# Kernel tuning notes

Measured on AMD Instinct MI355X. Metric: run time of the kernel, lower is better.

The kernel has to match this reference:

```python
import jax, jax.numpy as jnp
import numpy as np

N_NODES = 500_000
N_EDGES = 500_000
H = 128  # hidden_channels


def setup_inputs() -> dict:
    key = jax.random.key(0)
    k = jax.random.split(key, 8)
    z = jax.random.normal(k[0], (N_NODES, H), dtype=jnp.float32)
    edge_index = jax.random.randint(k[1], (2, N_EDGES), 0, N_NODES, dtype=jnp.int64)
    s1 = 1.0 / np.sqrt(4 * H)
    s2 = 1.0 / np.sqrt(H)
    s3 = 1.0 / np.sqrt(H // 2)
    W1 = jax.random.uniform(k[2], (4 * H, H), jnp.float32, -s1, s1)
    b1 = jax.random.uniform(k[3], (H,), jnp.float32, -s1, s1)
    W2 = jax.random.uniform(k[4], (H, H // 2), jnp.float32, -s2, s2)
    b2 = jax.random.uniform(k[5], (H // 2,), jnp.float32, -s2, s2)
    W3 = jax.random.uniform(k[6], (H // 2, 1), jnp.float32, -s3, s3)
    b3 = jax.random.uniform(k[7], (1,), jnp.float32, -s3, s3)
    return {"z": z, "edge_index": edge_index,
            "W1": W1, "b1": b1, "W2": W2, "b2": b2, "W3": W3, "b3": b3}


def reference(z, edge_index, W1, b1, W2, b2, W3, b3):
    # gather endpoint embeddings: [E, H]
    src = z[edge_index[0]]
    dst = z[edge_index[1]]
    interaction = src * dst
    difference = jnp.abs(src - dst)
    edge_repr = jnp.concatenate([src, dst, interaction, difference], axis=-1)  # [E, 4H]
    # MLP decoder (dropout = identity at eval)
    h = jax.nn.relu(edge_repr @ W1 + b1)
    h = jax.nn.relu(h @ W2 + b2)
    score = (h @ W3 + b3).squeeze(-1)  # [E]
    return score
```

## Files before the change

### kernel.cpp

```cpp
#include <hip/hip_runtime.h>
#include <stdint.h>


typedef __bf16 bf16x8 __attribute__((ext_vector_type(8)));
typedef __bf16 bf16x4 __attribute__((ext_vector_type(4)));
typedef float  f32x4  __attribute__((ext_vector_type(4)));

__device__ __forceinline__ short f2bf(float f) {
    union { float f; uint32_t u; } v; v.f = f;
    uint32_t u = v.u;
    uint32_t r = (u + 0x7fffu + ((u >> 16) & 1u)) >> 16;
    return (short)r;
}

__global__ void prep_kernel(const float* __restrict__ W1, const float* __restrict__ W2,
                            short* __restrict__ stage1, short* __restrict__ stage2) {
    int idx = blockIdx.x * 256 + threadIdx.x;
    if (idx < 65536) {
        int k = idx >> 7, n = idx & 127;
        float v = W1[idx];
        int ntile = n >> 4, ln = n & 15;
        int kstep = k >> 5, kr = k & 31;
        int lane = (kr >> 3) * 16 + ln;
        int j = kr & 7;
        stage1[(((ntile * 16 + kstep) * 64 + lane) << 3) + j] = f2bf(v);
    } else if (idx < 65536 + 8192) {
        int i2 = idx - 65536;
        int k = i2 >> 6, n = i2 & 63;
        float v = W2[i2];
        int ntile = n >> 4, ln = n & 15;
        int kstep = k >> 5, kr = k & 31;
        int lane = (kr >> 3) * 16 + ln;
        int j = kr & 7;
        stage2[(((ntile * 4 + kstep) * 64 + lane) << 3) + j] = f2bf(v);
    }
}

__launch_bounds__(256, 4)
__global__ void link_kernel(const float* __restrict__ z,
                            const int*   __restrict__ ei,
                            const float* __restrict__ b1,
                            const float* __restrict__ b2,
                            const float* __restrict__ w3,
                            const float* __restrict__ b3,
                            const short* __restrict__ stage1,
                            const short* __restrict__ stage2,
                            float* __restrict__ out,
                            int E) {
    __shared__ __align__(16) char smem[32768];

    const int tid  = threadIdx.x;
    const int lane = tid & 63;
    const int wave = tid >> 6;
    const int ln15 = lane & 15;
    const int quad = lane >> 4;
    const int e0   = blockIdx.x * 64;

    const int c    = tid & 31;
    const int mrow = tid >> 5;
    int si[8], di[8];
    #pragma unroll
    for (int i = 0; i < 8; ++i) {
        int eg = e0 + mrow + i * 8;
        int egc = eg < E ? eg : (E - 1);
        si[i] = ei[egc];
        di[i] = ei[E + egc];
    }
    f32x4 sv[8], dv[8];
    #pragma unroll
    for (int i = 0; i < 8; ++i) {
        sv[i] = *(const f32x4*)(z + (size_t)si[i] * 128 + c * 4);
        dv[i] = *(const f32x4*)(z + (size_t)di[i] * 128 + c * 4);
    }
    const int cc   = c >> 1;
    const int half = c & 1;
    #pragma unroll
    for (int i = 0; i < 8; ++i) {
        int m = mrow + i * 8;
        int addr = m * 256 + ((cc ^ (m & 15)) << 4) + half * 8;
        bf16x4 ps, pd;
        #pragma unroll
        for (int j = 0; j < 4; ++j) { ps[j] = (__bf16)sv[i][j]; pd[j] = (__bf16)dv[i][j]; }
        *(bf16x4*)(smem + addr)         = ps;
        *(bf16x4*)(smem + 16384 + addr) = pd;
    }
    __syncthreads();

    f32x4 acc[4][2];
    #pragma unroll
    for (int mt = 0; mt < 4; ++mt)
        #pragma unroll
        for (int nt = 0; nt < 2; ++nt)
            acc[mt][nt] = (f32x4){0.f, 0.f, 0.f, 0.f};

    #pragma unroll
    for (int ks4 = 0; ks4 < 4; ++ks4) {
        bf16x8 Bs[2], Bd[2];
        #pragma unroll
        for (int nt = 0; nt < 2; ++nt) {
            int ntile = wave * 2 + nt;
            Bs[nt] = *(const bf16x8*)(stage1 + (((ntile * 16 + 0 + ks4) * 64 + lane) << 3));
            Bd[nt] = *(const bf16x8*)(stage1 + (((ntile * 16 + 4 + ks4) * 64 + lane) << 3));
        }
        #pragma unroll
        for (int mt = 0; mt < 4; ++mt) {
            int m = mt * 16 + ln15;
            int off = m * 256 + (((ks4 * 4 + quad) ^ (m & 15)) << 4);
            bf16x8 sf = *(const bf16x8*)(smem + off);
            bf16x8 df = *(const bf16x8*)(smem + 16384 + off);
            #pragma unroll
            for (int nt = 0; nt < 2; ++nt) {
                acc[mt][nt] = __builtin_amdgcn_mfma_f32_16x16x32_bf16(sf, Bs[nt], acc[mt][nt], 0, 0, 0);
                acc[mt][nt] = __builtin_amdgcn_mfma_f32_16x16x32_bf16(df, Bd[nt], acc[mt][nt], 0, 0, 0);
            }
        }
    }
    __syncthreads();

    {
        int mder = wave * 16 + ln15;
        #pragma unroll
        for (int ks4 = 0; ks4 < 4; ++ks4) {
            int addr = mder * 256 + (((ks4 * 4 + quad) ^ ln15) << 4);
            bf16x8 s = *(const bf16x8*)(smem + addr);
            bf16x8 d = *(const bf16x8*)(smem + 16384 + addr);
            bf16x8 it, dd;
            #pragma unroll
            for (int j = 0; j < 8; ++j) {
                float fs = (float)s[j], fd = (float)d[j];
                it[j] = (__bf16)(fs * fd);
                dd[j] = (__bf16)__builtin_fabsf(fs - fd);
            }
            *(bf16x8*)(smem + addr)         = it;
            *(bf16x8*)(smem + 16384 + addr) = dd;
        }
    }
    __syncthreads();

    #pragma unroll
    for (int ks4 = 0; ks4 < 4; ++ks4) {
        bf16x8 Bi[2], Bf[2];
        #pragma unroll
        for (int nt = 0; nt < 2; ++nt) {
            int ntile = wave * 2 + nt;
            Bi[nt] = *(const bf16x8*)(stage1 + (((ntile * 16 +  8 + ks4) * 64 + lane) << 3));
            Bf[nt] = *(const bf16x8*)(stage1 + (((ntile * 16 + 12 + ks4) * 64 + lane) << 3));
        }
        #pragma unroll
        for (int mt = 0; mt < 4; ++mt) {
            int m = mt * 16 + ln15;
            int off = m * 256 + (((ks4 * 4 + quad) ^ (m & 15)) << 4);
            bf16x8 itf = *(const bf16x8*)(smem + off);
            bf16x8 ddf = *(const bf16x8*)(smem + 16384 + off);
            #pragma unroll
            for (int nt = 0; nt < 2; ++nt) {
                acc[mt][nt] = __builtin_amdgcn_mfma_f32_16x16x32_bf16(itf, Bi[nt], acc[mt][nt], 0, 0, 0);
                acc[mt][nt] = __builtin_amdgcn_mfma_f32_16x16x32_bf16(ddf, Bf[nt], acc[mt][nt], 0, 0, 0);
            }
        }
    }
    __syncthreads();

    #pragma unroll
    for (int nt = 0; nt < 2; ++nt) {
        int n = (wave * 2 + nt) * 16 + ln15;
        float bias = b1[n];
        #pragma unroll
        for (int mt = 0; mt < 4; ++mt) {
            #pragma unroll
            for (int r = 0; r < 4; ++r) {
                int row = mt * 16 + quad * 4 + r;
                float h = acc[mt][nt][r] + bias;
                h = h > 0.f ? h : 0.f;
                int addr = row * 256 + (((n >> 3) ^ (row & 15)) << 4) + (n & 7) * 2;
                *(short*)(smem + addr) = f2bf(h);
            }
        }
    }
    __syncthreads();

    f32x4 acc2[4];
    #pragma unroll
    for (int mt = 0; mt < 4; ++mt) acc2[mt] = (f32x4){0.f, 0.f, 0.f, 0.f};

    #pragma unroll
    for (int ks = 0; ks < 4; ++ks) {
        bf16x8 b = *(const bf16x8*)(stage2 + (((wave * 4 + ks) * 64 + lane) << 3));
        #pragma unroll
        for (int mt = 0; mt < 4; ++mt) {
            int m = mt * 16 + ln15;
            int ccr = ks * 4 + quad;
            bf16x8 a = *(const bf16x8*)(smem + m * 256 + ((ccr ^ (m & 15)) << 4));
            acc2[mt] = __builtin_amdgcn_mfma_f32_16x16x32_bf16(a, b, acc2[mt], 0, 0, 0);
        }
    }
    __syncthreads();

    {
        int n2 = wave * 16 + ln15;
        float bias = b2[n2];
        #pragma unroll
        for (int mt = 0; mt < 4; ++mt) {
            #pragma unroll
            for (int r = 0; r < 4; ++r) {
                int row = mt * 16 + quad * 4 + r;
                float h = acc2[mt][r] + bias;
                h = h > 0.f ? h : 0.f;
                *(float*)(smem + row * 272 + n2 * 4) = h;
            }
        }
    }
    __syncthreads();

    if (wave == 0) {
        int e = lane;
        float accf = b3[0];
        const float* h2p = (const float*)(smem + e * 272);
        #pragma unroll
        for (int kk = 0; kk < 16; ++kk) {
            f32x4 h = *(const f32x4*)(h2p + kk * 4);
            f32x4 w = *(const f32x4*)(w3 + kk * 4);
            accf += h[0] * w[0] + h[1] * w[1] + h[2] * w[2] + h[3] * w[3];
        }
        if (e0 + e < E) out[e0 + e] = accf;
    }
}

extern "C" void kernel_launch(void* const* d_in, const int* in_sizes, int n_in,
                              void* d_out, int out_size, void* d_ws, size_t ws_size,
                              hipStream_t stream) {
    const float* z  = (const float*)d_in[0];
    const int*   ei = (const int*)  d_in[1];
    const float* W1 = (const float*)d_in[2];
    const float* b1 = (const float*)d_in[3];
    const float* W2 = (const float*)d_in[4];
    const float* b2 = (const float*)d_in[5];
    const float* W3 = (const float*)d_in[6];
    const float* b3 = (const float*)d_in[7];
    float* out = (float*)d_out;

    int E = in_sizes[1] / 2;

    short* stage1 = (short*)d_ws;
    short* stage2 = stage1 + 65536;

    prep_kernel<<<288, 256, 0, stream>>>(W1, W2, stage1, stage2);

    int nblk = (E + 63) / 64;
    link_kernel<<<nblk, 256, 0, stream>>>(z, ei, b1, b2, W3, b3, stage1, stage2, out, E);
}
```

Measured before the change: 415.3 us.

## Make link kernel persistent and prefetch next tile's gathers during compute

The edge MLP kernel becomes a persistent grid-stride loop over 64-edge tiles, launched with at most 768 blocks. While the current tile is being computed, it loads the next tile's edge indices and gathers its endpoint embeddings into registers, so gather latency overlaps MFMA work. Biases and W3 are cached in shared memory, and some syncthreads calls become explicit waitcnt plus barrier. This raises register pressure, which is why the occupancy hint drops from 4 to 3 blocks per CU, and fewer resident waves are left to hide latency.

Measured after the change: 939.2 us. 2.26x slower.

```diff
diff --git a/kernel.cpp b/kernel.cpp
--- a/kernel.cpp
+++ b/kernel.cpp
@@ -36,7 +36,7 @@
     }
 }
 
-__launch_bounds__(256, 4)
+__launch_bounds__(256, 3)
 __global__ void link_kernel(const float* __restrict__ z,
                             const int*   __restrict__ ei,
                             const float* __restrict__ b1,
@@ -46,183 +46,228 @@
                             const short* __restrict__ stage1,
                             const short* __restrict__ stage2,
                             float* __restrict__ out,
-                            int E) {
+                            int E, int ntiles) {
     __shared__ __align__(16) char smem[32768];
+    __shared__ __align__(16) float sbias[260];
 
     const int tid  = threadIdx.x;
     const int lane = tid & 63;
     const int wave = tid >> 6;
     const int ln15 = lane & 15;
     const int quad = lane >> 4;
-    const int e0   = blockIdx.x * 64;
+    const int G    = gridDim.x;
+
+    if (tid < 128)      sbias[tid] = b1[tid];
+    else if (tid < 192) sbias[tid] = b2[tid - 128];
+    else                sbias[tid] = w3[tid - 192];
+    if (tid == 0) sbias[256] = b3[0];
 
     const int c    = tid & 31;
     const int mrow = tid >> 5;
-    int si[8], di[8];
-    #pragma unroll
-    for (int i = 0; i < 8; ++i) {
-        int eg = e0 + mrow + i * 8;
-        int egc = eg < E ? eg : (E - 1);
-        si[i] = ei[egc];
-        di[i] = ei[E + egc];
-    }
-    f32x4 sv[8], dv[8];
-    #pragma unroll
-    for (int i = 0; i < 8; ++i) {
-        sv[i] = *(const f32x4*)(z + (size_t)si[i] * 128 + c * 4);
-        dv[i] = *(const f32x4*)(z + (size_t)di[i] * 128 + c * 4);
-    }
     const int cc   = c >> 1;
     const int half = c & 1;
-    #pragma unroll
-    for (int i = 0; i < 8; ++i) {
-        int m = mrow + i * 8;
-        int addr = m * 256 + ((cc ^ (m & 15)) << 4) + half * 8;
-        bf16x4 ps, pd;
-        #pragma unroll
-        for (int j = 0; j < 4; ++j) { ps[j] = (__bf16)sv[i][j]; pd[j] = (__bf16)dv[i][j]; }
-        *(bf16x4*)(smem + addr)         = ps;
-        *(bf16x4*)(smem + 16384 + addr) = pd;
+
+    int si[8], di[8];
+    f32x4 sv[8], dv[8];
+
+    int T = blockIdx.x;
+    {
+        int e0 = T * 64;
+        #pragma unroll
+        for (int i = 0; i < 8; ++i) {
+            int eg = e0 + mrow + i * 8;
+            int egc = eg < E ? eg : (E - 1);
+            si[i] = ei[egc];
+            di[i] = ei[E + egc];
+        }
+        #pragma unroll
+        for (int i = 0; i < 8; ++i) {
+            sv[i] = *(const f32x4*)(z + (size_t)si[i] * 128 + c * 4);
+            dv[i] = *(const f32x4*)(z + (size_t)di[i] * 128 + c * 4);
+        }
     }
-    __syncthreads();
-
-    f32x4 acc[4][2];
-    #pragma unroll
-    for (int mt = 0; mt < 4; ++mt)
-        #pragma unroll
-        for (int nt = 0; nt < 2; ++nt)
-            acc[mt][nt] = (f32x4){0.f, 0.f, 0.f, 0.f};
-
-    #pragma unroll
-    for (int ks4 = 0; ks4 < 4; ++ks4) {
-        bf16x8 Bs[2], Bd[2];
+
+    for (; T < ntiles; T += G) {
+        const int e0 = T * 64;
+        const bool hasNext = (T + G) < ntiles;
+
+        #pragma unroll
+        for (int i = 0; i < 8; ++i) {
+            int m = mrow + i * 8;
+            int addr = m * 256 + ((cc ^ (m & 15)) << 4) + half * 8;
+            bf16x4 ps, pd;
+            #pragma unroll
+            for (int j = 0; j < 4; ++j) { ps[j] = (__bf16)sv[i][j]; pd[j] = (__bf16)dv[i][j]; }
+            *(bf16x4*)(smem + addr)         = ps;
+            *(bf16x4*)(smem + 16384 + addr) = pd;
+        }
+        __syncthreads();
+
+        if (hasNext) {
+            int en0 = (T + G) * 64;
+            #pragma unroll
+            for (int i = 0; i < 8; ++i) {
+                int eg = en0 + mrow + i * 8;
+                int egc = eg < E ? eg : (E - 1);
+                si[i] = ei[egc];
+                di[i] = ei[E + egc];
+            }
+        }
+
+        f32x4 acc[4][2];
+        #pragma unroll
+        for (int mt = 0; mt < 4; ++mt)
+            #pragma unroll
+            for (int nt = 0; nt < 2; ++nt)
+                acc[mt][nt] = (f32x4){0.f, 0.f, 0.f, 0.f};
+
+        #pragma unroll
+        for (int ks4 = 0; ks4 < 4; ++ks4) {
+            bf16x8 Bs[2], Bd[2];
+            #pragma unroll
+            for (int nt = 0; nt < 2; ++nt) {
+                int ntile = wave * 2 + nt;
+                Bs[nt] = *(const bf16x8*)(stage1 + (((ntile * 16 + 0 + ks4) * 64 + lane) << 3));
+                Bd[nt] = *(const bf16x8*)(stage1 + (((ntile * 16 + 4 + ks4) * 64 + lane) << 3));
+            }
+            #pragma unroll
+            for (int mt = 0; mt < 4; ++mt) {
+                int m = mt * 16 + ln15;
+                int off = m * 256 + (((ks4 * 4 + quad) ^ (m & 15)) << 4);
+                bf16x8 sf = *(const bf16x8*)(smem + off);
+                bf16x8 df = *(const bf16x8*)(smem + 16384 + off);
+                #pragma unroll
+                for (int nt = 0; nt < 2; ++nt) {
+                    acc[mt][nt] = __builtin_amdgcn_mfma_f32_16x16x32_bf16(sf, Bs[nt], acc[mt][nt], 0, 0, 0);
+                    acc[mt][nt] = __builtin_amdgcn_mfma_f32_16x16x32_bf16(df, Bd[nt], acc[mt][nt], 0, 0, 0);
+                }
+            }
+        }
+        __syncthreads();
+
+        {
+            int mder = wave * 16 + ln15;
+            #pragma unroll
+            for (int ks4 = 0; ks4 < 4; ++ks4) {
+                int addr = mder * 256 + (((ks4 * 4 + quad) ^ ln15) << 4);
+                bf16x8 s = *(const bf16x8*)(smem + addr);
+                bf16x8 d = *(const bf16x8*)(smem + 16384 + addr);
+                bf16x8 it, dd;
+                #pragma unroll
+                for (int j = 0; j < 8; ++j) {
+                    float fs = (float)s[j], fd = (float)d[j];
+                    it[j] = (__bf16)(fs * fd);
+                    dd[j] = (__bf16)__builtin_fabsf(fs - fd);
+                }
+                *(bf16x8*)(smem + addr)         = it;
+                *(bf16x8*)(smem + 16384 + addr) = dd;
+            }
+        }
+        __syncthreads();
+
+        #pragma unroll
+        for (int ks4 = 0; ks4 < 4; ++ks4) {
+            bf16x8 Bi[2], Bf[2];
+            #pragma unroll
+            for (int nt = 0; nt < 2; ++nt) {
+                int ntile = wave * 2 + nt;
+                Bi[nt] = *(const bf16x8*)(stage1 + (((ntile * 16 +  8 + ks4) * 64 + lane) << 3));
+                Bf[nt] = *(const bf16x8*)(stage1 + (((ntile * 16 + 12 + ks4) * 64 + lane) << 3));
+            }
+            #pragma unroll
+            for (int mt = 0; mt < 4; ++mt) {
+                int m = mt * 16 + ln15;
+                int off = m * 256 + (((ks4 * 4 + quad) ^ (m & 15)) << 4);
+                bf16x8 itf = *(const bf16x8*)(smem + off);
+                bf16x8 ddf = *(const bf16x8*)(smem + 16384 + off);
+                #pragma unroll
+                for (int nt = 0; nt < 2; ++nt) {
+                    acc[mt][nt] = __builtin_amdgcn_mfma_f32_16x16x32_bf16(itf, Bi[nt], acc[mt][nt], 0, 0, 0);
+                    acc[mt][nt] = __builtin_amdgcn_mfma_f32_16x16x32_bf16(ddf, Bf[nt], acc[mt][nt], 0, 0, 0);
+                }
+            }
+        }
+        __syncthreads();
+
         #pragma unroll
         for (int nt = 0; nt < 2; ++nt) {
-            int ntile = wave * 2 + nt;
-            Bs[nt] = *(const bf16x8*)(stage1 + (((ntile * 16 + 0 + ks4) * 64 + lane) << 3));
-            Bd[nt] = *(const bf16x8*)(stage1 + (((ntile * 16 + 4 + ks4) * 64 + lane) << 3));
-        }
-        #pragma unroll
-        for (int mt = 0; mt < 4; ++mt) {
-            int m = mt * 16 + ln15;
-            int off = m * 256 + (((ks4 * 4 + quad) ^ (m & 15)) << 4);
-            bf16x8 sf = *(const bf16x8*)(smem + off);
-            bf16x8 df = *(const bf16x8*)(smem + 16384 + off);
-            #pragma unroll
-            for (int nt = 0; nt < 2; ++nt) {
-                acc[mt][nt] = __builtin_amdgcn_mfma_f32_16x16x32_bf16(sf, Bs[nt], acc[mt][nt], 0, 0, 0);
-                acc[mt][nt] = __builtin_amdgcn_mfma_f32_16x16x32_bf16(df, Bd[nt], acc[mt][nt], 0, 0, 0);
-            }
-        }
-    }
-    __syncthreads();
-
-    {
-        int mder = wave * 16 + ln15;
-        #pragma unroll
-        for (int ks4 = 0; ks4 < 4; ++ks4) {
-            int addr = mder * 256 + (((ks4 * 4 + quad) ^ ln15) << 4);
-            bf16x8 s = *(const bf16x8*)(smem + addr);
-            bf16x8 d = *(const bf16x8*)(smem + 16384 + addr);
-            bf16x8 it, dd;
-            #pragma unroll
-            for (int j = 0; j < 8; ++j) {
-                float fs = (float)s[j], fd = (float)d[j];
-                it[j] = (__bf16)(fs * fd);
-                dd[j] = (__bf16)__builtin_fabsf(fs - fd);
-            }
-            *(bf16x8*)(smem + addr)         = it;
-            *(bf16x8*)(smem + 16384 + addr) = dd;
-        }
-    }
-    __syncthreads();
-
-    #pragma unroll
-    for (int ks4 = 0; ks4 < 4; ++ks4) {
-        bf16x8 Bi[2], Bf[2];
-        #pragma unroll
-        for (int nt = 0; nt < 2; ++nt) {
-            int ntile = wave * 2 + nt;
-            Bi[nt] = *(const bf16x8*)(stage1 + (((ntile * 16 +  8 + ks4) * 64 + lane) << 3));
-            Bf[nt] = *(const bf16x8*)(stage1 + (((ntile * 16 + 12 + ks4) * 64 + lane) << 3));
-        }
-        #pragma unroll
-        for (int mt = 0; mt < 4; ++mt) {
-            int m = mt * 16 + ln15;
-            int off = m * 256 + (((ks4 * 4 + quad) ^ (m & 15)) << 4);
-            bf16x8 itf = *(const bf16x8*)(smem + off);
-            bf16x8 ddf = *(const bf16x8*)(smem + 16384 + off);
-            #pragma unroll
-            for (int nt = 0; nt < 2; ++nt) {
-                acc[mt][nt] = __builtin_amdgcn_mfma_f32_16x16x32_bf16(itf, Bi[nt], acc[mt][nt], 0, 0, 0);
-                acc[mt][nt] = __builtin_amdgcn_mfma_f32_16x16x32_bf16(ddf, Bf[nt], acc[mt][nt], 0, 0, 0);
-            }
-        }
-    }
-    __syncthreads();
-
-    #pragma unroll
-    for (int nt = 0; nt < 2; ++nt) {
-        int n = (wave * 2 + nt) * 16 + ln15;
-        float bias = b1[n];
-        #pragma unroll
-        for (int mt = 0; mt < 4; ++mt) {
-            #pragma unroll
-            for (int r = 0; r < 4; ++r) {
-                int row = mt * 16 + quad * 4 + r;
-                float h = acc[mt][nt][r] + bias;
-                h = h > 0.f ? h : 0.f;
-                int addr = row * 256 + (((n >> 3) ^ (row & 15)) << 4) + (n & 7) * 2;
-                *(short*)(smem + addr) = f2bf(h);
-            }
-        }
-    }
-    __syncthreads();
-
-    f32x4 acc2[4];
-    #pragma unroll
-    for (int mt = 0; mt < 4; ++mt) acc2[mt] = (f32x4){0.f, 0.f, 0.f, 0.f};
-
-    #pragma unroll
-    for (int ks = 0; ks < 4; ++ks) {
-        bf16x8 b = *(const bf16x8*)(stage2 + (((wave * 4 + ks) * 64 + lane) << 3));
-        #pragma unroll
-        for (int mt = 0; mt < 4; ++mt) {
-            int m = mt * 16 + ln15;
-            int ccr = ks * 4 + quad;
-            bf16x8 a = *(const bf16x8*)(smem + m * 256 + ((ccr ^ (m & 15)) << 4));
-            acc2[mt] = __builtin_amdgcn_mfma_f32_16x16x32_bf16(a, b, acc2[mt], 0, 0, 0);
-        }
-    }
-    __syncthreads();
-
-    {
-        int n2 = wave * 16 + ln15;
-        float bias = b2[n2];
-        #pragma unroll
-        for (int mt = 0; mt < 4; ++mt) {
-            #pragma unroll
-            for (int r = 0; r < 4; ++r) {
-                int row = mt * 16 + quad * 4 + r;
-                float h = acc2[mt][r] + bias;
-                h = h > 0.f ? h : 0.f;
-                *(float*)(smem + row * 272 + n2 * 4) = h;
-            }
-        }
-    }
-    __syncthreads();
-
-    if (wave == 0) {
-        int e = lane;
-        float accf = b3[0];
-        const float* h2p = (const float*)(smem + e * 272);
-        #pragma unroll
-        for (int kk = 0; kk < 16; ++kk) {
-            f32x4 h = *(const f32x4*)(h2p + kk * 4);
-            f32x4 w = *(const f32x4*)(w3 + kk * 4);
-            accf += h[0] * w[0] + h[1] * w[1] + h[2] * w[2] + h[3] * w[3];
-        }
-        if (e0 + e < E) out[e0 + e] = accf;
+            int n = (wave * 2 + nt) * 16 + ln15;
+            float bias = sbias[n];
+            #pragma unroll
+            for (int mt = 0; mt < 4; ++mt) {
+                #pragma unroll
+                for (int r = 0; r < 4; ++r) {
+                    int row = mt * 16 + quad * 4 + r;
+                    float h = acc[mt][nt][r] + bias;
+                    h = h > 0.f ? h : 0.f;
+                    int addr = row * 256 + (((n >> 3) ^ (row & 15)) << 4) + (n & 7) * 2;
+                    *(short*)(smem + addr) = f2bf(h);
+                }
+            }
+        }
+        __syncthreads();
+
+        f32x4 acc2[4];
+        #pragma unroll
+        for (int mt = 0; mt < 4; ++mt) acc2[mt] = (f32x4){0.f, 0.f, 0.f, 0.f};
+
+        bf16x8 b2frag[4];
+        #pragma unroll
+        for (int ks = 0; ks < 4; ++ks)
+            b2frag[ks] = *(const bf16x8*)(stage2 + (((wave * 4 + ks) * 64 + lane) << 3));
+
+        if (hasNext) {
+            #pragma unroll
+            for (int i = 0; i < 8; ++i) {
+                sv[i] = *(const f32x4*)(z + (size_t)si[i] * 128 + c * 4);
+                dv[i] = *(const f32x4*)(z + (size_t)di[i] * 128 + c * 4);
+            }
+        }
+
+        #pragma unroll
+        for (int ks = 0; ks < 4; ++ks) {
+            #pragma unroll
+            for (int mt = 0; mt < 4; ++mt) {
+                int m = mt * 16 + ln15;
+                int ccr = ks * 4 + quad;
+                bf16x8 a = *(const bf16x8*)(smem + m * 256 + ((ccr ^ (m & 15)) << 4));
+                acc2[mt] = __builtin_amdgcn_mfma_f32_16x16x32_bf16(a, b2frag[ks], acc2[mt], 0, 0, 0);
+            }
+        }
+        asm volatile("s_waitcnt lgkmcnt(0)" ::: "memory");
+        __builtin_amdgcn_s_barrier();
+
+        {
+            int n2 = wave * 16 + ln15;
+            float bias = sbias[128 + n2];
+            #pragma unroll
+            for (int mt = 0; mt < 4; ++mt) {
+                #pragma unroll
+                for (int r = 0; r < 4; ++r) {
+                    int row = mt * 16 + quad * 4 + r;
+                    float h = acc2[mt][r] + bias;
+                    h = h > 0.f ? h : 0.f;
+                    *(float*)(smem + row * 272 + n2 * 4) = h;
+                }
+            }
+        }
+        asm volatile("s_waitcnt lgkmcnt(0)" ::: "memory");
+        __builtin_amdgcn_s_barrier();
+
+        if (wave == 0) {
+            int e = lane;
+            float accf = sbias[256];
+            const float* h2p = (const float*)(smem + e * 272);
+            #pragma unroll
+            for (int kk = 0; kk < 16; ++kk) {
+                f32x4 h = *(const f32x4*)(h2p + kk * 4);
+                f32x4 w = *(const f32x4*)(&sbias[192 + kk * 4]);
+                accf += h[0] * w[0] + h[1] * w[1] + h[2] * w[2] + h[3] * w[3];
+            }
+            if (e0 + e < E) out[e0 + e] = accf;
+        }
+        asm volatile("s_waitcnt lgkmcnt(0)" ::: "memory");
+        __builtin_amdgcn_s_barrier();
     }
 }
 
@@ -246,6 +291,8 @@
 
     prep_kernel<<<288, 256, 0, stream>>>(W1, W2, stage1, stage2);
 
-    int nblk = (E + 63) / 64;
-    link_kernel<<<nblk, 256, 0, stream>>>(z, ei, b1, b2, W3, b3, stage1, stage2, out, E);
-}
+    int ntiles = (E + 63) / 64;
+    int nblk = ntiles < 768 ? ntiles : 768;
+    link_kernel<<<nblk, 256, 0, stream>>>(z, ei, b1, b2, W3, b3, stage1, stage2,
+                                          out, E, ntiles);
+}
```
